# Performance work log

Measured on AMD Instinct MI355X. Metric: run time of the kernel, lower is better.

Reference implementation:

```python
import jax, jax.numpy as jnp
import numpy as np

D_MODEL = 512
N_HEADS = 8
D_KEYS = D_MODEL // N_HEADS  # 64
DIN = D_MODEL * 2            # 1024
DPROJ = D_KEYS * N_HEADS * 2 # 1024
B, L = 2, 2048


def setup_inputs() -> dict:
    key = jax.random.key(0)
    ks = jax.random.split(key, 11)
    s_in = 1.0 / np.sqrt(DIN)
    s_out = 1.0 / np.sqrt(DPROJ)
    return {
        "queries": jax.random.normal(ks[0], (B, L, DIN), jnp.float32),
        "keys": jax.random.normal(ks[1], (B, L, DIN), jnp.float32),
        "values": jax.random.normal(ks[2], (B, L, DIN), jnp.float32),
        "Wq": jax.random.normal(ks[3], (DPROJ, DIN), jnp.float32) * s_in,
        "bq": jax.random.normal(ks[4], (DPROJ,), jnp.float32) * s_in,
        "Wk": jax.random.normal(ks[5], (DPROJ, DIN), jnp.float32) * s_in,
        "bk": jax.random.normal(ks[6], (DPROJ,), jnp.float32) * s_in,
        "Wv": jax.random.normal(ks[7], (DPROJ, DIN), jnp.float32) * s_in,
        "bv": jax.random.normal(ks[8], (DPROJ,), jnp.float32) * s_in,
        "Wo": jax.random.normal(ks[9], (DIN, DPROJ), jnp.float32) * s_out,
        "bo": jax.random.normal(ks[10], (DIN,), jnp.float32) * s_out,
    }


def reference(queries, keys, values, Wq, bq, Wk, bk, Wv, bv, Wo, bo):
    b, l, _ = queries.shape
    H, E = N_HEADS, 2
    # projections: (B, L, DIN) -> (B, L, d_keys, H, 2)
    q = (queries @ Wq.T + bq).reshape(b, l, -1, H, E)
    k = (keys @ Wk.T + bk).reshape(b, l, -1, H, E)
    v = (values @ Wv.T + bv).reshape(b, l, -1, H, E)
    scale = 1.0 / np.sqrt(E)  # E=2 (real/imag)
    # attention over the d_keys axis, per token n, per head h
    scores = jnp.einsum('bnlhe,bnshe->bnhls', q, k)  # (B, L, H, dk, dk)
    A = jax.nn.softmax(scale * scores, axis=-1)
    out = jnp.einsum('bnhls,bnshd->bnlhd', A, v)     # (B, L, dk, H, 2)
    out = out.reshape(b, l, -1)                      # (B, L, dk*H*2)
    return out @ Wo.T + bo                           # (B, L, 2*d_model)
```

## Files before the change

### kernel.cpp

```cpp
#include <hip/hip_runtime.h>
#include <hip/hip_bf16.h>
#include <stdint.h>

#define TOK   4096
#define KDIM  1024
#define NDIM  1024
#define NHEAD 8

typedef _Float16 f16;
typedef __attribute__((ext_vector_type(2))) _Float16 h2;
typedef __attribute__((ext_vector_type(8))) _Float16 f16x8;
typedef __attribute__((ext_vector_type(4))) float f32x4;
typedef __attribute__((ext_vector_type(4))) uint u32x4;

__device__ __forceinline__ void gload_lds16(const void* g, void* l) {
    __builtin_amdgcn_global_load_lds(
        (const __attribute__((address_space(1))) void*)g,
        (__attribute__((address_space(3))) void*)l, 16, 0, 0);
}


struct CvtArgs {
    const float* src[7];
    void*        dst[7];
    int          n4[7];
    int          type[7];
};

__global__ __launch_bounds__(256) void cvt_kernel(CvtArgs a) {
    const int seg = blockIdx.y;
    const int type = a.type[seg];
    const float4* s = (const float4*)a.src[seg];
    const int n4 = a.n4[seg];
    const int stride = gridDim.x * blockDim.x;
    for (int i = blockIdx.x * blockDim.x + threadIdx.x; i < n4; i += stride) {
        float4 v = s[i];
        if (type == 0) {
            f16* d = (f16*)a.dst[seg];
            union { f16 h[4]; uint2 u; } o;
            o.h[0] = (f16)v.x; o.h[1] = (f16)v.y; o.h[2] = (f16)v.z; o.h[3] = (f16)v.w;
            *(uint2*)(d + (size_t)i * 4) = o.u;
        } else if (type == 1) {
            f16* d = (f16*)a.dst[seg];
            const int r = i >> 8, c = (i & 255) * 4;
            const int rp = ((r >> 1) & 7) * 128 + (r >> 4) * 2 + (r & 1);
            union { f16 h[4]; uint2 u; } o;
            o.h[0] = (f16)v.x; o.h[1] = (f16)v.y; o.h[2] = (f16)v.z; o.h[3] = (f16)v.w;
            *(uint2*)(d + (size_t)rp * 1024 + c) = o.u;
        } else {
            f16* d = (f16*)a.dst[seg];
            const int r = i >> 8, c = (i & 255) * 4;
            const int p0 = ((c >> 1) & 7) * 128 + (c >> 4) * 2;
            const int p1 = (((c + 2) >> 1) & 7) * 128 + ((c + 2) >> 4) * 2;
            union { f16 h[2]; uint u; } u01, u23;
            u01.h[0] = (f16)v.x; u01.h[1] = (f16)v.y;
            u23.h[0] = (f16)v.z; u23.h[1] = (f16)v.w;
            *(uint*)(d + (size_t)r * 1024 + p0) = u01.u;
            *(uint*)(d + (size_t)r * 1024 + p1) = u23.u;
        }
    }
}

struct GemmArgs {
    const f16*   A[3];
    const f16*   B[3];
    const float* bias[3];
    void*        C[3];
};

#define VM_WAIT4 asm volatile("s_waitcnt vmcnt(4)" ::: "memory")
#define VM_WAIT0 asm volatile("s_waitcnt vmcnt(0)" ::: "memory")

template<int OUTMODE>
__global__ __launch_bounds__(512) void gemm_bt_kernel(GemmArgs ga) {
    constexpr int K = KDIM, N = NDIM;
    constexpr int NT = K / 64;
    const f16*   A    = ga.A[blockIdx.z];
    const f16*   B    = ga.B[blockIdx.z];
    const float* bias = ga.bias[blockIdx.z];

    __shared__ f16 sm[2 * (128 * 64 + 128 * 64)];

    const int tid  = threadIdx.x;
    const int wave = tid >> 6, lane = tid & 63;
    const int wm = wave >> 2, wn = wave & 3;
    const int bm = blockIdx.x * 128, bn = blockIdx.y * 128;
    const int lrow = lane & 15, kgrp = lane >> 4;

    f32x4 acc[4][2] = {};

    const int srow = tid >> 3;
    const int colL = (tid & 7) << 3;
    const int colG = (((tid & 7) ^ (srow & 7)) << 3);

    auto stage = [&](int buf, int kt) {
        f16* As = sm + buf * (128 * 64 + 128 * 64);
        f16* Bs = As + 128 * 64;
        #pragma unroll
        for (int i = 0; i < 2; ++i) {
            const int row = srow + i * 64;
            gload_lds16(A + (size_t)(bm + row) * K + kt + colG, As + row * 64 + colL);
        }
        #pragma unroll
        for (int i = 0; i < 2; ++i) {
            const int row = srow + i * 64;
            gload_lds16(B + (size_t)(bn + row) * K + kt + colG, Bs + row * 64 + colL);
        }
    };

    stage(0, 0);

    const int swz = (lrow & 7) << 3;

    for (int it = 0; it < NT; ++it) {
        const int cur = it & 1;
        if (it + 1 < NT) {
            stage(cur ^ 1, (it + 1) * 64);
            VM_WAIT4;
        } else {
            VM_WAIT0;
        }
        __builtin_amdgcn_s_barrier();
        __builtin_amdgcn_sched_barrier(0);

        const f16* As = sm + cur * (128 * 64 + 128 * 64);
        const f16* Bs = As + 128 * 64;
        #pragma unroll
        for (int kk = 0; kk < 2; ++kk) {
            f16x8 af[4], bf[2];
            const int kcol = (kk * 32 + kgrp * 8) ^ swz;
            #pragma unroll
            for (int mi = 0; mi < 4; ++mi)
                af[mi] = *(const f16x8*)(As + (wm * 64 + mi * 16 + lrow) * 64 + kcol);
            #pragma unroll
            for (int ni = 0; ni < 2; ++ni)
                bf[ni] = *(const f16x8*)(Bs + (wn * 32 + ni * 16 + lrow) * 64 + kcol);
            #pragma unroll
            for (int mi = 0; mi < 4; ++mi)
                #pragma unroll
                for (int ni = 0; ni < 2; ++ni)
                    acc[mi][ni] = __builtin_amdgcn_mfma_f32_16x16x32_f16(af[mi], bf[ni], acc[mi][ni], 0, 0, 0);
        }
        __builtin_amdgcn_s_barrier();
    }

    const int rbase = kgrp * 4;
    #pragma unroll
    for (int mi = 0; mi < 4; ++mi) {
        #pragma unroll
        for (int ni = 0; ni < 2; ++ni) {
            const int col = bn + wn * 32 + ni * 16 + lrow;
            const int bidx = (OUTMODE == 0)
                ? (((col >> 1) & 63) * 16 + (col >> 7) * 2 + (col & 1))
                : col;
            const float bv = bias[bidx];
            #pragma unroll
            for (int r = 0; r < 4; ++r) {
                const int row = bm + wm * 64 + mi * 16 + rbase + r;
                const float v = acc[mi][ni][r] + bv;
                if constexpr (OUTMODE == 0)
                    ((f16*)ga.C[blockIdx.z])[(size_t)row * N + col] = (f16)v;
                else
                    ((float*)ga.C[blockIdx.z])[(size_t)row * N + col] = v;
            }
        }
    }
}

__global__ __launch_bounds__(256) void attn_kernel(const f16* qp, const f16* kp,
                                                   const f16* vp, f16* ao) {
    const int tid = threadIdx.x, wave = tid >> 6, lane = tid & 63;
    const int task = blockIdx.x * 4 + wave;
    const size_t base = (size_t)task * 64;
    const float SCALE = 0.70710678118f * 1.44269504089f;

    union U2 { uint u; h2 h; f16 s[2]; };
    U2 qu; qu.u = ((const uint*)qp)[base + lane];
    const float q0 = (float)qu.s[0] * SCALE, q1 = (float)qu.s[1] * SCALE;
#if __has_builtin(__builtin_amdgcn_fdot2)
    h2 qs; qs[0] = (f16)q0; qs[1] = (f16)q1;
#endif

    const u32x4* kb = (const u32x4*)((const uint*)kp + base);
    const u32x4* vb = (const u32x4*)((const uint*)vp + base);

    float sum = 0.f, o0 = 0.f, o1 = 0.f;
    #pragma unroll
    for (int g = 0; g < 4; ++g) {
        u32x4 kr[4], vr[4];
        #pragma unroll
        for (int i = 0; i < 4; ++i) { kr[i] = kb[g * 4 + i]; vr[i] = vb[g * 4 + i]; }
        #pragma unroll
        for (int i = 0; i < 4; ++i) {
            #pragma unroll
            for (int j = 0; j < 4; ++j) {
                U2 ku, vu;
                ku.u = kr[i][j];
                vu.u = vr[i][j];
#if __has_builtin(__builtin_amdgcn_fdot2)
                const float sc = __builtin_amdgcn_fdot2(qs, ku.h, 0.0f, false);
#else
                const float sc = fmaf(q0, (float)ku.s[0], q1 * (float)ku.s[1]);
#endif
                const float p = exp2f(sc);
                sum += p;
                o0 = fmaf(p, (float)vu.s[0], o0);
                o1 = fmaf(p, (float)vu.s[1], o1);
            }
        }
    }
    const float inv = __builtin_amdgcn_rcpf(sum);
    U2 o;
    o.s[0] = (f16)(o0 * inv);
    o.s[1] = (f16)(o1 * inv);
    ((uint*)ao)[base + lane] = o.u;
}

extern "C" void kernel_launch(void* const* d_in, const int* in_sizes, int n_in,
                              void* d_out, int out_size, void* d_ws, size_t ws_size,
                              hipStream_t stream) {
    const float* queries = (const float*)d_in[0];
    const float* keys    = (const float*)d_in[1];
    const float* values  = (const float*)d_in[2];
    const float* Wq = (const float*)d_in[3];
    const float* bq = (const float*)d_in[4];
    const float* Wk = (const float*)d_in[5];
    const float* bk = (const float*)d_in[6];
    const float* Wv = (const float*)d_in[7];
    const float* bv = (const float*)d_in[8];
    const float* Wo = (const float*)d_in[9];
    const float* bo = (const float*)d_in[10];

    char* ws = (char*)d_ws;
    const size_t MB = 1024 * 1024;
    f16* Xq  = (f16*)(ws + 0 * MB);
    f16* Xk  = (f16*)(ws + 8 * MB);
    f16* Xv  = (f16*)(ws + 16 * MB);
    f16* Wqh = (f16*)(ws + 24 * MB);
    f16* Wkh = (f16*)(ws + 26 * MB);
    f16* Wvh = (f16*)(ws + 28 * MB);
    f16* Woh = (f16*)(ws + 30 * MB);
    f16* qp  = (f16*)(ws + 32 * MB);
    f16* kp  = (f16*)(ws + 40 * MB);
    f16* vp  = (f16*)(ws + 48 * MB);
    f16* ao  = (f16*)(ws + 56 * MB);

    CvtArgs ca;
    ca.src[0] = queries; ca.dst[0] = Xq;  ca.n4[0] = TOK * KDIM / 4;  ca.type[0] = 0;
    ca.src[1] = keys;    ca.dst[1] = Xk;  ca.n4[1] = TOK * KDIM / 4;  ca.type[1] = 0;
    ca.src[2] = values;  ca.dst[2] = Xv;  ca.n4[2] = TOK * KDIM / 4;  ca.type[2] = 0;
    ca.src[3] = Wq;      ca.dst[3] = Wqh; ca.n4[3] = NDIM * KDIM / 4; ca.type[3] = 1;
    ca.src[4] = Wk;      ca.dst[4] = Wkh; ca.n4[4] = NDIM * KDIM / 4; ca.type[4] = 1;
    ca.src[5] = Wv;      ca.dst[5] = Wvh; ca.n4[5] = NDIM * KDIM / 4; ca.type[5] = 1;
    ca.src[6] = Wo;      ca.dst[6] = Woh; ca.n4[6] = NDIM * KDIM / 4; ca.type[6] = 2;
    cvt_kernel<<<dim3(256, 7), 256, 0, stream>>>(ca);

    GemmArgs g1;
    g1.A[0] = Xq;  g1.A[1] = Xk;  g1.A[2] = Xv;
    g1.B[0] = Wqh; g1.B[1] = Wkh; g1.B[2] = Wvh;
    g1.bias[0] = bq; g1.bias[1] = bk; g1.bias[2] = bv;
    g1.C[0] = qp; g1.C[1] = kp; g1.C[2] = vp;
    gemm_bt_kernel<0><<<dim3(32, 8, 3), 512, 0, stream>>>(g1);

    attn_kernel<<<TOK * NHEAD / 4, 256, 0, stream>>>(qp, kp, vp, ao);

    GemmArgs g2;
    g2.A[0] = ao; g2.B[0] = Woh; g2.bias[0] = bo; g2.C[0] = d_out;
    g2.A[1] = ao; g2.B[1] = Woh; g2.bias[1] = bo; g2.C[1] = d_out;
    g2.A[2] = ao; g2.B[2] = Woh; g2.bias[2] = bo; g2.C[2] = d_out;
    gemm_bt_kernel<1><<<dim3(32, 8, 1), 512, 0, stream>>>(g2);
}
```

Before: 215.0 us.

## Store V projection in fp32 and use packed FMA with raw exp2 in attention

The QKV GEMM now writes the V projection as fp32 instead of fp16, and the attention kernel reads V as float4 vectors. This removes the per-element fp16-to-fp32 converts so the two output accumulations can use a packed float2 FMA. The exp2 call becomes the hardware exp2 builtin, and the softmax sum is split into two accumulators to shorten the dependency chain. In exchange V-projection stores and attention V loads move twice as many bytes, and the workspace layout shifts to make room.

New measurement: 218.3 us. About the same (+1.5%).

```diff
diff --git a/kernel.cpp b/kernel.cpp
--- a/kernel.cpp
+++ b/kernel.cpp
@@ -10,8 +10,15 @@
 typedef _Float16 f16;
 typedef __attribute__((ext_vector_type(2))) _Float16 h2;
 typedef __attribute__((ext_vector_type(8))) _Float16 f16x8;
+typedef __attribute__((ext_vector_type(2))) float f32x2;
 typedef __attribute__((ext_vector_type(4))) float f32x4;
 typedef __attribute__((ext_vector_type(4))) uint u32x4;
+
+#if __has_builtin(__builtin_amdgcn_exp2f)
+#define EXP2(x) __builtin_amdgcn_exp2f(x)
+#else
+#define EXP2(x) exp2f(x)
+#endif
 
 __device__ __forceinline__ void gload_lds16(const void* g, void* l) {
     __builtin_amdgcn_global_load_lds(
@@ -158,17 +165,21 @@
             for (int r = 0; r < 4; ++r) {
                 const int row = bm + wm * 64 + mi * 16 + rbase + r;
                 const float v = acc[mi][ni][r] + bv;
-                if constexpr (OUTMODE == 0)
-                    ((f16*)ga.C[blockIdx.z])[(size_t)row * N + col] = (f16)v;
-                else
+                if constexpr (OUTMODE == 0) {
+                    if (blockIdx.z == 2)
+                        ((float*)ga.C[2])[(size_t)row * N + col] = v;
+                    else
+                        ((f16*)ga.C[blockIdx.z])[(size_t)row * N + col] = (f16)v;
+                } else {
                     ((float*)ga.C[blockIdx.z])[(size_t)row * N + col] = v;
+                }
             }
         }
     }
 }
 
 __global__ __launch_bounds__(256) void attn_kernel(const f16* qp, const f16* kp,
-                                                   const f16* vp, f16* ao) {
+                                                   const float* vp, f16* ao) {
     const int tid = threadIdx.x, wave = tid >> 6, lane = tid & 63;
     const int task = blockIdx.x * 4 + wave;
     const size_t base = (size_t)task * 64;
@@ -182,37 +193,36 @@
 #endif
 
     const u32x4* kb = (const u32x4*)((const uint*)kp + base);
-    const u32x4* vb = (const u32x4*)((const uint*)vp + base);
-
-    float sum = 0.f, o0 = 0.f, o1 = 0.f;
+    const f32x4* vb = (const f32x4*)(vp + base * 2);
+
+    f32x2 o01 = {0.f, 0.f};
+    float sum0 = 0.f, sum1 = 0.f;
     #pragma unroll
     for (int g = 0; g < 4; ++g) {
-        u32x4 kr[4], vr[4];
-        #pragma unroll
-        for (int i = 0; i < 4; ++i) { kr[i] = kb[g * 4 + i]; vr[i] = vb[g * 4 + i]; }
-        #pragma unroll
-        for (int i = 0; i < 4; ++i) {
-            #pragma unroll
-            for (int j = 0; j < 4; ++j) {
-                U2 ku, vu;
-                ku.u = kr[i][j];
-                vu.u = vr[i][j];
+        u32x4 kr[4];
+        f32x4 vr[8];
+        #pragma unroll
+        for (int i = 0; i < 4; ++i) kr[i] = kb[g * 4 + i];
+        #pragma unroll
+        for (int i = 0; i < 8; ++i) vr[i] = vb[g * 8 + i];
+        #pragma unroll
+        for (int s = 0; s < 16; ++s) {
+            U2 ku; ku.u = kr[s >> 2][s & 3];
 #if __has_builtin(__builtin_amdgcn_fdot2)
-                const float sc = __builtin_amdgcn_fdot2(qs, ku.h, 0.0f, false);
+            const float sc = __builtin_amdgcn_fdot2(qs, ku.h, 0.0f, false);
 #else
-                const float sc = fmaf(q0, (float)ku.s[0], q1 * (float)ku.s[1]);
+            const float sc = fmaf(q0, (float)ku.s[0], q1 * (float)ku.s[1]);
 #endif
-                const float p = exp2f(sc);
-                sum += p;
-                o0 = fmaf(p, (float)vu.s[0], o0);
-                o1 = fmaf(p, (float)vu.s[1], o1);
-            }
-        }
-    }
-    const float inv = __builtin_amdgcn_rcpf(sum);
+            const float p = EXP2(sc);
+            if (s & 1) sum1 += p; else sum0 += p;
+            const f32x2 v2 = {vr[s >> 1][(s & 1) << 1], vr[s >> 1][((s & 1) << 1) + 1]};
+            o01 = __builtin_elementwise_fma((f32x2){p, p}, v2, o01);
+        }
+    }
+    const float inv = __builtin_amdgcn_rcpf(sum0 + sum1);
     U2 o;
-    o.s[0] = (f16)(o0 * inv);
-    o.s[1] = (f16)(o1 * inv);
+    o.s[0] = (f16)(o01.x * inv);
+    o.s[1] = (f16)(o01.y * inv);
     ((uint*)ao)[base + lane] = o.u;
 }
 
@@ -233,17 +243,17 @@
 
     char* ws = (char*)d_ws;
     const size_t MB = 1024 * 1024;
-    f16* Xq  = (f16*)(ws + 0 * MB);
-    f16* Xk  = (f16*)(ws + 8 * MB);
-    f16* Xv  = (f16*)(ws + 16 * MB);
-    f16* Wqh = (f16*)(ws + 24 * MB);
-    f16* Wkh = (f16*)(ws + 26 * MB);
-    f16* Wvh = (f16*)(ws + 28 * MB);
-    f16* Woh = (f16*)(ws + 30 * MB);
-    f16* qp  = (f16*)(ws + 32 * MB);
-    f16* kp  = (f16*)(ws + 40 * MB);
-    f16* vp  = (f16*)(ws + 48 * MB);
-    f16* ao  = (f16*)(ws + 56 * MB);
+    f16*   Xq   = (f16*)(ws + 0 * MB);
+    f16*   Xk   = (f16*)(ws + 8 * MB);
+    f16*   Xv   = (f16*)(ws + 16 * MB);
+    f16*   Wqh  = (f16*)(ws + 24 * MB);
+    f16*   Wkh  = (f16*)(ws + 26 * MB);
+    f16*   Wvh  = (f16*)(ws + 28 * MB);
+    f16*   Woh  = (f16*)(ws + 30 * MB);
+    f16*   qp   = (f16*)(ws + 32 * MB);
+    f16*   kp   = (f16*)(ws + 40 * MB);
+    float* vp32 = (float*)(ws + 48 * MB);
+    f16*   ao   = (f16*)(ws + 64 * MB);
 
     CvtArgs ca;
     ca.src[0] = queries; ca.dst[0] = Xq;  ca.n4[0] = TOK * KDIM / 4;  ca.type[0] = 0;
@@ -259,10 +269,10 @@
     g1.A[0] = Xq;  g1.A[1] = Xk;  g1.A[2] = Xv;
     g1.B[0] = Wqh; g1.B[1] = Wkh; g1.B[2] = Wvh;
     g1.bias[0] = bq; g1.bias[1] = bk; g1.bias[2] = bv;
-    g1.C[0] = qp; g1.C[1] = kp; g1.C[2] = vp;
+    g1.C[0] = qp; g1.C[1] = kp; g1.C[2] = vp32;
     gemm_bt_kernel<0><<<dim3(32, 8, 3), 512, 0, stream>>>(g1);
 
-    attn_kernel<<<TOK * NHEAD / 4, 256, 0, stream>>>(qp, kp, vp, ao);
+    attn_kernel<<<TOK * NHEAD / 4, 256, 0, stream>>>(qp, kp, vp32, ao);
 
     GemmArgs g2;
     g2.A[0] = ao; g2.B[0] = Woh; g2.bias[0] = bo; g2.C[0] = d_out;
```
